# Kernel optimization log

Measured on AMD Instinct MI355X. Metric: run time of the kernel, lower is better.

Reference implementation:

```python
import jax, jax.numpy as jnp
import numpy as np

N, D, K = 8192, 4096, 8
F_HID = D // 4  # 1024


def setup_inputs() -> dict:
    key = jax.random.key(0)
    ks = jax.random.split(key, 8)
    s1 = 1.0 / np.sqrt(2 * D)
    s2 = 1.0 / np.sqrt(F_HID)
    sr = 1.0 / np.sqrt(D)
    return {
        "h_anchor": jax.random.normal(ks[0], (N, D), jnp.float32),
        "h_mask": jax.random.normal(ks[1], (N, D), jnp.float32),
        "Wr": jax.random.normal(ks[2], (K, D), jnp.float32) * sr,
        "br": jnp.zeros((K,), jnp.float32),
        "W1": jax.random.normal(ks[3], (K, F_HID, 2 * D), jnp.float32) * s1,
        "b1": jnp.zeros((K, F_HID), jnp.float32),
        "W2": jax.random.normal(ks[4], (K, D, F_HID), jnp.float32) * s2,
        "b2": jnp.zeros((K, D), jnp.float32),
    }


def reference(h_anchor, h_mask, Wr, br, W1, b1, W2, b2):
    # routing weights: softmax(h_mask @ Wr^T + br) -> [N, K]
    weights = jax.nn.softmax(h_mask @ Wr.T + br, axis=-1)
    # conditioned input: [N, 2D]
    conditioned = jnp.concatenate([h_anchor, h_mask], axis=-1)
    # all-expert first GEMM: [K, N, F]
    h1 = jnp.einsum("nc,kfc->knf", conditioned, W1) + b1[:, None, :]
    h1 = jax.nn.gelu(h1, approximate=False)  # torch nn.GELU default = exact erf
    # second GEMM: [K, N, D]
    expert_out = jnp.einsum("knf,kdf->knd", h1, W2) + b2[:, None, :]
    # softmax-weighted combine over experts -> [N, D]
    return jnp.einsum("knd,nk->nd", expert_out, weights)
```

## Files before the change

### kernel.cpp

```cpp
#include <hip/hip_runtime.h>
#include <hip/hip_bf16.h>
#include <math.h>

typedef __bf16 bf16_t;
typedef __bf16 bf16x4 __attribute__((ext_vector_type(4)));
typedef __bf16 bf16x8 __attribute__((ext_vector_type(8)));
typedef float  f32x4  __attribute__((ext_vector_type(4)));

#define AS1 __attribute__((address_space(1)))
#define AS3 __attribute__((address_space(3)))

__device__ __forceinline__ void gload_lds16(const bf16_t* g, char* l) {
  __builtin_amdgcn_global_load_lds((const AS1 void*)g, (AS3 void*)l, 16, 0, 0);
}

static constexpr int N_ROWS = 8192;
static constexpr int DDIM   = 4096;
static constexpr int KEXP   = 8;
static constexpr int FHID   = 1024;
static constexpr int KD     = 8192;
static constexpr int NKT64  = KD / 64;
static constexpr int NKT32  = KD / 32;


__global__ __launch_bounds__(256)
void routing_kernel(const float* __restrict__ hm, const float* __restrict__ Wr,
                    const float* __restrict__ br, float* __restrict__ wgt) {
  const int n = blockIdx.x;
  const int t = threadIdx.x;
  const int wid = t >> 6;
  const float4* row = (const float4*)(hm + (size_t)n * DDIM);
  float4 x[4];
#pragma unroll
  for (int j = 0; j < 4; ++j) x[j] = row[t + j * 256];
  __shared__ float red[KEXP][4];
  float part[KEXP];
#pragma unroll
  for (int k = 0; k < KEXP; ++k) {
    const float4* wr = (const float4*)(Wr + (size_t)k * DDIM);
    float s = 0.f;
#pragma unroll
    for (int j = 0; j < 4; ++j) {
      float4 w4 = wr[t + j * 256];
      s += x[j].x * w4.x + x[j].y * w4.y + x[j].z * w4.z + x[j].w * w4.w;
    }
#pragma unroll
    for (int off = 32; off > 0; off >>= 1) s += __shfl_down(s, off);
    part[k] = s;
  }
  if ((t & 63) == 0) {
#pragma unroll
    for (int k = 0; k < KEXP; ++k) red[k][wid] = part[k];
  }
  __syncthreads();
  if (t == 0) {
    float lg[KEXP];
    float mx = -1e30f;
#pragma unroll
    for (int k = 0; k < KEXP; ++k) {
      lg[k] = red[k][0] + red[k][1] + red[k][2] + red[k][3] + br[k];
      mx = fmaxf(mx, lg[k]);
    }
    float sum = 0.f;
#pragma unroll
    for (int k = 0; k < KEXP; ++k) { lg[k] = expf(lg[k] - mx); sum += lg[k]; }
    float inv = 1.f / sum;
#pragma unroll
    for (int k = 0; k < KEXP; ++k) wgt[(size_t)n * KEXP + k] = lg[k] * inv;
  }
}

__device__ __forceinline__ bf16x4 cvt4(float4 v) {
  bf16x4 o;
  o[0] = (bf16_t)v.x; o[1] = (bf16_t)v.y; o[2] = (bf16_t)v.z; o[3] = (bf16_t)v.w;
  return o;
}

__global__ __launch_bounds__(256)
void pack_cond_kernel(const float* __restrict__ ha, const float* __restrict__ hm,
                      bf16_t* __restrict__ Apk) {
  const int bm = blockIdx.x >> 7, t = blockIdx.x & 127;
  const int tid = threadIdx.x;
  const float* src = (t < 64) ? ha : hm;
  const int cb = (t & 63) * 64;
  __shared__ char pb[32768];
#pragma unroll
  for (int i = 0; i < 16; ++i) {
    int u = i * 256 + tid;
    int r = u >> 4, c = (u & 15) * 4;
    float4 v = *(const float4*)(src + (size_t)(bm * 256 + r) * DDIM + cb + c);
    int off = ((r >> 7) & 1) * 16384 + ((c >> 4) & 3) * 4096 + ((r >> 5) & 3) * 1024
            + ((c >> 3) & 1) * 512 + (r & 31) * 16 + (c & 7) * 2;
    *(bf16x4*)(pb + off) = cvt4(v);
  }
  __syncthreads();
  char* dst = (char*)Apk + (size_t)blockIdx.x * 32768;
#pragma unroll
  for (int i = 0; i < 8; ++i) {
    int off = i * 4096 + tid * 16;
    *(float4*)(dst + off) = *(const float4*)(pb + off);
  }
}

__global__ __launch_bounds__(256)
void pack_w1_kernel(const float* __restrict__ W1, bf16_t* __restrict__ Bpk) {
  const int bn = blockIdx.x >> 7, t = blockIdx.x & 127;
  const int tid = threadIdx.x;
  __shared__ char pb[32768];
#pragma unroll
  for (int i = 0; i < 16; ++i) {
    int u = i * 256 + tid;
    int r = u >> 4, c = (u & 15) * 4;
    float4 v = *(const float4*)(W1 + (size_t)(bn * 256 + r) * KD + t * 64 + c);
    int off = ((c >> 4) & 3) * 8192 + ((r >> 5) & 7) * 1024
            + ((c >> 3) & 1) * 512 + (r & 31) * 16 + (c & 7) * 2;
    *(bf16x4*)(pb + off) = cvt4(v);
  }
  __syncthreads();
  char* dst = (char*)Bpk + (size_t)blockIdx.x * 32768;
#pragma unroll
  for (int i = 0; i < 8; ++i) {
    int off = i * 4096 + tid * 16;
    *(float4*)(dst + off) = *(const float4*)(pb + off);
  }
}

__global__ __launch_bounds__(256)
void pack_w2_kernel(const float* __restrict__ W2, bf16_t* __restrict__ Bpk) {
  const int bn = blockIdx.x >> 7, t = blockIdx.x & 127;
  const int tid = threadIdx.x;
  const int ke = t >> 4, f0 = (t & 15) * 64;
  __shared__ char pb[32768];
#pragma unroll
  for (int i = 0; i < 16; ++i) {
    int u = i * 256 + tid;
    int r = u >> 4, c = (u & 15) * 4;
    float4 v = *(const float4*)(W2 + ((size_t)ke * DDIM + bn * 256 + r) * FHID + f0 + c);
    int off = ((c >> 4) & 3) * 8192 + ((r >> 5) & 7) * 1024
            + ((c >> 3) & 1) * 512 + (r & 31) * 16 + (c & 7) * 2;
    *(bf16x4*)(pb + off) = cvt4(v);
  }
  __syncthreads();
  char* dst = (char*)Bpk + (size_t)blockIdx.x * 32768;
#pragma unroll
  for (int i = 0; i < 8; ++i) {
    int off = i * 4096 + tid * 16;
    *(float4*)(dst + off) = *(const float4*)(pb + off);
  }
}

template <int MODE, int NCOLS>
__global__ __launch_bounds__(512, 4)
void gemm_kernel(const bf16_t* __restrict__ Apk, const bf16_t* __restrict__ Bpk,
                 void* __restrict__ Cout, const float* __restrict__ bias,
                 const float* __restrict__ wgt) {
  __shared__ char lds[3 * 24576];

  const int tid  = threadIdx.x;
  const int wid  = tid >> 6;
  const int lane = tid & 63;
  const int wr   = wid >> 1;
  const int wc   = wid & 1;

  constexpr int NBN    = NCOLS / 128;
  constexpr int NWIN_N = NBN / 16;
  const int bid = blockIdx.x;
  const int w   = bid >> 8;
  const int sl  = bid & 255;
  const int xcd = sl & 7;
  const int cu  = sl >> 3;
  const int wm  = w / NWIN_N, wn = w % NWIN_N;
  const int bm  = wm * 16 + ((xcd >> 1) << 2) + (cu & 3);
  const int bn  = wn * 16 + ((xcd & 1) << 3) + (cu >> 2);
  const int arow0 = bm * 256;
  const int bcol0 = bn * 128;

  const char* Abase = (const char*)Apk + (size_t)bm * NKT64 * 32768;
  const char* Bbase = (const char*)Bpk + (size_t)(bn >> 1) * NKT64 * 32768;
  const int pA0 = 2 * wid, pA1 = 2 * wid + 1, qB = wid;
  const int a0s = (pA0 >> 3) * 16384 + ((pA0 >> 2) & 1) * 4096 + (pA0 & 3) * 1024;
  const int a1s = (pA1 >> 3) * 16384 + ((pA1 >> 2) & 1) * 4096 + (pA1 & 3) * 1024;
  const int a0d = (pA0 >> 3) * 8192 + ((pA0 >> 2) & 1) * 4096 + (pA0 & 3) * 1024;
  const int a1d = (pA1 >> 3) * 8192 + ((pA1 >> 2) & 1) * 4096 + (pA1 & 3) * 1024;
  const int bqs = (qB >> 2) * 8192 + ((bn & 1) * 4 + (qB & 3)) * 1024;
  const int bqd = 16384 + (qB >> 2) * 4096 + (qB & 3) * 1024;

  const int lpart = (lane & 15) * 16 + ((lane >> 4) & 1) * 512 + (lane >> 5) * 4096;
  int aoff[4], boff[4];
#pragma unroll
  for (int mi = 0; mi < 4; ++mi)
    aoff[mi] = (wr >> 1) * 8192 + ((wr & 1) * 2 + (mi >> 1)) * 1024 + (mi & 1) * 256 + lpart;
#pragma unroll
  for (int nj = 0; nj < 4; ++nj)
    boff[nj] = 16384 + (wc * 2 + (nj >> 1)) * 1024 + (nj & 1) * 256 + lpart;

  f32x4 acc[4][4];
  f32x4 zero = {0.f, 0.f, 0.f, 0.f};
#pragma unroll
  for (int mi = 0; mi < 4; ++mi)
#pragma unroll
    for (int nj = 0; nj < 4; ++nj) acc[mi][nj] = zero;

#define SB __builtin_amdgcn_sched_barrier(0);
#define STG3(KT, BUF)                                                            \
  {                                                                              \
    const int kt_ = (KT) & (NKT32 - 1);                                          \
    const size_t t64 = (size_t)(kt_ >> 1) * 32768;                               \
    const int klo = (kt_ & 1) * 2;                                               \
    gload_lds16((const bf16_t*)(Abase + t64 + a0s + klo * 4096 + lane * 16),     \
                (BUF) + a0d);                                                    \
    gload_lds16((const bf16_t*)(Abase + t64 + a1s + klo * 4096 + lane * 16),     \
                (BUF) + a1d);                                                    \
    gload_lds16((const bf16_t*)(Bbase + t64 + bqs + klo * 8192 + lane * 16),     \
                (BUF) + bqd);                                                    \
  }

  STG3(0, lds) STG3(1, lds + 24576) SB
  asm volatile("s_waitcnt vmcnt(3)" ::: "memory");
  SB
  __builtin_amdgcn_s_barrier();
  SB

  char* rb = lds;
  char* mb = lds + 24576;
  char* sb = lds + 49152;

#pragma unroll 1
  for (int t = 0; t < NKT32; ++t) {
    STG3(t + 2, sb) SB
    bf16x8 a0, a1, a2, a3, b0, b1, b2, b3;
    a0 = *(const bf16x8*)(rb + aoff[0]); SB
    a1 = *(const bf16x8*)(rb + aoff[1]); SB
    a2 = *(const bf16x8*)(rb + aoff[2]); SB
    a3 = *(const bf16x8*)(rb + aoff[3]); SB
    b0 = *(const bf16x8*)(rb + boff[0]); SB
    b1 = *(const bf16x8*)(rb + boff[1]); SB
    b2 = *(const bf16x8*)(rb + boff[2]); SB
    b3 = *(const bf16x8*)(rb + boff[3]); SB
    __builtin_amdgcn_s_setprio(1);
    asm volatile("s_waitcnt lgkmcnt(3)" ::: "memory"); SB
    acc[0][0] = __builtin_amdgcn_mfma_f32_16x16x32_bf16(a0, b0, acc[0][0], 0, 0, 0);
    acc[1][0] = __builtin_amdgcn_mfma_f32_16x16x32_bf16(a1, b0, acc[1][0], 0, 0, 0);
    acc[2][0] = __builtin_amdgcn_mfma_f32_16x16x32_bf16(a2, b0, acc[2][0], 0, 0, 0);
    acc[3][0] = __builtin_amdgcn_mfma_f32_16x16x32_bf16(a3, b0, acc[3][0], 0, 0, 0);
    SB
    asm volatile("s_waitcnt lgkmcnt(2)" ::: "memory"); SB
    acc[0][1] = __builtin_amdgcn_mfma_f32_16x16x32_bf16(a0, b1, acc[0][1], 0, 0, 0);
    acc[1][1] = __builtin_amdgcn_mfma_f32_16x16x32_bf16(a1, b1, acc[1][1], 0, 0, 0);
    acc[2][1] = __builtin_amdgcn_mfma_f32_16x16x32_bf16(a2, b1, acc[2][1], 0, 0, 0);
    acc[3][1] = __builtin_amdgcn_mfma_f32_16x16x32_bf16(a3, b1, acc[3][1], 0, 0, 0);
    SB
    asm volatile("s_waitcnt lgkmcnt(1)" ::: "memory"); SB
    acc[0][2] = __builtin_amdgcn_mfma_f32_16x16x32_bf16(a0, b2, acc[0][2], 0, 0, 0);
    acc[1][2] = __builtin_amdgcn_mfma_f32_16x16x32_bf16(a1, b2, acc[1][2], 0, 0, 0);
    acc[2][2] = __builtin_amdgcn_mfma_f32_16x16x32_bf16(a2, b2, acc[2][2], 0, 0, 0);
    acc[3][2] = __builtin_amdgcn_mfma_f32_16x16x32_bf16(a3, b2, acc[3][2], 0, 0, 0);
    SB
    asm volatile("s_waitcnt lgkmcnt(0)" ::: "memory"); SB
    acc[0][3] = __builtin_amdgcn_mfma_f32_16x16x32_bf16(a0, b3, acc[0][3], 0, 0, 0);
    acc[1][3] = __builtin_amdgcn_mfma_f32_16x16x32_bf16(a1, b3, acc[1][3], 0, 0, 0);
    acc[2][3] = __builtin_amdgcn_mfma_f32_16x16x32_bf16(a2, b3, acc[2][3], 0, 0, 0);
    acc[3][3] = __builtin_amdgcn_mfma_f32_16x16x32_bf16(a3, b3, acc[3][3], 0, 0, 0);
    SB
    __builtin_amdgcn_s_setprio(0);
    asm volatile("s_waitcnt vmcnt(3)" ::: "memory");
    SB
    __builtin_amdgcn_s_barrier();
    SB
    char* tmp = rb; rb = mb; mb = sb; sb = tmp;
  }
#undef STG3
#undef SB

  const int rbase = arow0 + wr * 64 + ((lane >> 4) << 2);
  const int cbase = bcol0 + wc * 64 + (lane & 15);

  if constexpr (MODE == 1) {
    char* __restrict__ Hc = (char*)Cout;
    const int kexp = bcol0 >> 10;
    float bv[4];
    size_t cpart[4];
#pragma unroll
    for (int nj = 0; nj < 4; ++nj) {
      int c = cbase + nj * 16;
      bv[nj] = bias[c];
      cpart[nj] = (size_t)(c >> 6) * 32768 + ((c >> 4) & 3) * 4096
                + ((c >> 3) & 1) * 512 + (c & 7) * 2;
    }
#pragma unroll
    for (int mi = 0; mi < 4; ++mi)
#pragma unroll
      for (int r = 0; r < 4; ++r) {
        int n = rbase + mi * 16 + r;
        float wn4 = wgt[(size_t)n * KEXP + kexp];
        size_t npart = (size_t)(n >> 8) * (NKT64 * 32768) + ((n >> 7) & 1) * 16384
                     + ((n >> 5) & 3) * 1024 + (n & 31) * 16;
#pragma unroll
        for (int nj = 0; nj < 4; ++nj) {
          float x = acc[mi][nj][r] + bv[nj];
          float g = 0.5f * x * (1.f + erff(x * 0.70710678118654752f));
          *(bf16_t*)(Hc + npart + cpart[nj]) = (bf16_t)(g * wn4);
        }
      }
  } else {
    float* __restrict__ O = (float*)Cout;
    float bc[4][KEXP];
#pragma unroll
    for (int nj = 0; nj < 4; ++nj)
#pragma unroll
      for (int k = 0; k < KEXP; ++k)
        bc[nj][k] = bias[(size_t)k * NCOLS + cbase + nj * 16];
#pragma unroll
    for (int mi = 0; mi < 4; ++mi)
#pragma unroll
      for (int r = 0; r < 4; ++r) {
        int n = rbase + mi * 16 + r;
        const float4* wp = (const float4*)(wgt + (size_t)n * KEXP);
        float4 wa = wp[0], wb = wp[1];
        float w8[KEXP] = {wa.x, wa.y, wa.z, wa.w, wb.x, wb.y, wb.z, wb.w};
#pragma unroll
        for (int nj = 0; nj < 4; ++nj) {
          float s = 0.f;
#pragma unroll
          for (int k = 0; k < KEXP; ++k) s += w8[k] * bc[nj][k];
          O[(size_t)n * NCOLS + cbase + nj * 16] = acc[mi][nj][r] + s;
        }
      }
  }
}

extern "C" void kernel_launch(void* const* d_in, const int* in_sizes, int n_in,
                              void* d_out, int out_size, void* d_ws, size_t ws_size,
                              hipStream_t stream) {
  const float* h_anchor = (const float*)d_in[0];
  const float* h_mask   = (const float*)d_in[1];
  const float* Wr       = (const float*)d_in[2];
  const float* br       = (const float*)d_in[3];
  const float* W1       = (const float*)d_in[4];
  const float* b1       = (const float*)d_in[5];
  const float* W2       = (const float*)d_in[6];
  const float* b2       = (const float*)d_in[7];
  float* out = (float*)d_out;

  char* ws = (char*)d_ws;
  bf16_t* Apk  = (bf16_t*)(ws);
  bf16_t* B1pk = (bf16_t*)(ws + ((size_t)128 << 20));
  bf16_t* B2pk = (bf16_t*)(ws + ((size_t)256 << 20));
  bf16_t* Hpk  = (bf16_t*)(ws + ((size_t)320 << 20));
  float*  wgt  = (float*) (ws + ((size_t)448 << 20));

  routing_kernel<<<N_ROWS, 256, 0, stream>>>(h_mask, Wr, br, wgt);
  pack_cond_kernel<<<32 * 128, 256, 0, stream>>>(h_anchor, h_mask, Apk);
  pack_w1_kernel<<<32 * 128, 256, 0, stream>>>(W1, B1pk);
  pack_w2_kernel<<<16 * 128, 256, 0, stream>>>(W2, B2pk);

  gemm_kernel<1, 8192><<<(N_ROWS / 256) * (KD / 128), 512, 0, stream>>>(
      Apk, B1pk, (void*)Hpk, b1, wgt);
  gemm_kernel<2, 4096><<<(N_ROWS / 256) * (DDIM / 128), 512, 0, stream>>>(
      Hpk, B2pk, (void*)out, b2, wgt);
}
```

Baseline: 1.611 ms.

## Repack operands into contiguous K32 tiles and unroll triple-buffer loop

Changes the packed bf16 layout of activations and weights so that each 32-wide K step is one contiguous 16 KB chunk. Global-to-LDS loads can then use a single incrementing pointer instead of per-iteration address arithmetic. The main loop is unrolled by three with fixed LDS buffer offsets, which removes the buffer-pointer rotation and the per-thread offset arrays. The intent is to cut scalar and vector address overhead in the hot loop, at the cost of larger code and a layout change that the packing kernels and the hidden-activation epilogue must all match exactly.

```diff
diff --git a/kernel.cpp b/kernel.cpp
--- a/kernel.cpp
+++ b/kernel.cpp
@@ -19,7 +19,6 @@
 static constexpr int KEXP   = 8;
 static constexpr int FHID   = 1024;
 static constexpr int KD     = 8192;
-static constexpr int NKT64  = KD / 64;
 static constexpr int NKT32  = KD / 32;
 
 
@@ -89,8 +88,8 @@
     int u = i * 256 + tid;
     int r = u >> 4, c = (u & 15) * 4;
     float4 v = *(const float4*)(src + (size_t)(bm * 256 + r) * DDIM + cb + c);
-    int off = ((r >> 7) & 1) * 16384 + ((c >> 4) & 3) * 4096 + ((r >> 5) & 3) * 1024
-            + ((c >> 3) & 1) * 512 + (r & 31) * 16 + (c & 7) * 2;
+    int off = (c >> 5) * 16384 + ((r >> 7) & 1) * 8192 + ((c >> 4) & 1) * 4096
+            + ((r >> 5) & 3) * 1024 + ((c >> 3) & 1) * 512 + (r & 31) * 16 + (c & 7) * 2;
     *(bf16x4*)(pb + off) = cvt4(v);
   }
   __syncthreads();
@@ -112,7 +111,7 @@
     int u = i * 256 + tid;
     int r = u >> 4, c = (u & 15) * 4;
     float4 v = *(const float4*)(W1 + (size_t)(bn * 256 + r) * KD + t * 64 + c);
-    int off = ((c >> 4) & 3) * 8192 + ((r >> 5) & 7) * 1024
+    int off = (c >> 5) * 16384 + ((c >> 4) & 1) * 8192 + ((r >> 5) & 7) * 1024
             + ((c >> 3) & 1) * 512 + (r & 31) * 16 + (c & 7) * 2;
     *(bf16x4*)(pb + off) = cvt4(v);
   }
@@ -136,7 +135,7 @@
     int u = i * 256 + tid;
     int r = u >> 4, c = (u & 15) * 4;
     float4 v = *(const float4*)(W2 + ((size_t)ke * DDIM + bn * 256 + r) * FHID + f0 + c);
-    int off = ((c >> 4) & 3) * 8192 + ((r >> 5) & 7) * 1024
+    int off = (c >> 5) * 16384 + ((c >> 4) & 1) * 8192 + ((r >> 5) & 7) * 1024
             + ((c >> 3) & 1) * 512 + (r & 31) * 16 + (c & 7) * 2;
     *(bf16x4*)(pb + off) = cvt4(v);
   }
@@ -175,24 +174,17 @@
   const int arow0 = bm * 256;
   const int bcol0 = bn * 128;
 
-  const char* Abase = (const char*)Apk + (size_t)bm * NKT64 * 32768;
-  const char* Bbase = (const char*)Bpk + (size_t)(bn >> 1) * NKT64 * 32768;
-  const int pA0 = 2 * wid, pA1 = 2 * wid + 1, qB = wid;
-  const int a0s = (pA0 >> 3) * 16384 + ((pA0 >> 2) & 1) * 4096 + (pA0 & 3) * 1024;
-  const int a1s = (pA1 >> 3) * 16384 + ((pA1 >> 2) & 1) * 4096 + (pA1 & 3) * 1024;
-  const int a0d = (pA0 >> 3) * 8192 + ((pA0 >> 2) & 1) * 4096 + (pA0 & 3) * 1024;
-  const int a1d = (pA1 >> 3) * 8192 + ((pA1 >> 2) & 1) * 4096 + (pA1 & 3) * 1024;
-  const int bqs = (qB >> 2) * 8192 + ((bn & 1) * 4 + (qB & 3)) * 1024;
-  const int bqd = 16384 + (qB >> 2) * 4096 + (qB & 3) * 1024;
+  const int pA0 = 2 * wid, qB = wid;
+  const char* pA = (const char*)Apk + (size_t)bm * NKT32 * 16384
+                 + pA0 * 1024 + lane * 16;
+  const char* pB = (const char*)Bpk + (size_t)(bn >> 1) * NKT32 * 16384
+                 + (qB >> 2) * 8192 + ((bn & 1) * 4 + (qB & 3)) * 1024 + lane * 16;
+  const int dA = pA0 * 1024;
+  const int dB = 16384 + qB * 1024;
 
   const int lpart = (lane & 15) * 16 + ((lane >> 4) & 1) * 512 + (lane >> 5) * 4096;
-  int aoff[4], boff[4];
-#pragma unroll
-  for (int mi = 0; mi < 4; ++mi)
-    aoff[mi] = (wr >> 1) * 8192 + ((wr & 1) * 2 + (mi >> 1)) * 1024 + (mi & 1) * 256 + lpart;
-#pragma unroll
-  for (int nj = 0; nj < 4; ++nj)
-    boff[nj] = 16384 + (wc * 2 + (nj >> 1)) * 1024 + (nj & 1) * 256 + lpart;
+  const char* pAr = lds + (wr >> 1) * 8192 + (wr & 1) * 2048 + lpart;
+  const char* pBr = lds + 16384 + wc * 2048 + lpart;
 
   f32x4 acc[4][4];
   f32x4 zero = {0.f, 0.f, 0.f, 0.f};
@@ -202,74 +194,71 @@
     for (int nj = 0; nj < 4; ++nj) acc[mi][nj] = zero;
 
 #define SB __builtin_amdgcn_sched_barrier(0);
-#define STG3(KT, BUF)                                                            \
+#define STG(SBOFF)                                                               \
+  gload_lds16((const bf16_t*)pA,          lds + (SBOFF) + dA);                   \
+  gload_lds16((const bf16_t*)(pA + 1024), lds + (SBOFF) + dA + 1024);            \
+  gload_lds16((const bf16_t*)pB,          lds + (SBOFF) + dB);                   \
+  pA += 16384; pB += 16384;
+
+#define BODY(RB, SBOFF)                                                          \
   {                                                                              \
-    const int kt_ = (KT) & (NKT32 - 1);                                          \
-    const size_t t64 = (size_t)(kt_ >> 1) * 32768;                               \
-    const int klo = (kt_ & 1) * 2;                                               \
-    gload_lds16((const bf16_t*)(Abase + t64 + a0s + klo * 4096 + lane * 16),     \
-                (BUF) + a0d);                                                    \
-    gload_lds16((const bf16_t*)(Abase + t64 + a1s + klo * 4096 + lane * 16),     \
-                (BUF) + a1d);                                                    \
-    gload_lds16((const bf16_t*)(Bbase + t64 + bqs + klo * 8192 + lane * 16),     \
-                (BUF) + bqd);                                                    \
-  }
-
-  STG3(0, lds) STG3(1, lds + 24576) SB
+    STG(SBOFF) SB                                                                \
+    bf16x8 a0, a1, a2, a3, b0, b1, b2, b3;                                       \
+    a0 = *(const bf16x8*)(pAr + (RB));          SB                               \
+    a1 = *(const bf16x8*)(pAr + (RB) + 256);    SB                               \
+    a2 = *(const bf16x8*)(pAr + (RB) + 1024);   SB                               \
+    a3 = *(const bf16x8*)(pAr + (RB) + 1280);   SB                               \
+    b0 = *(const bf16x8*)(pBr + (RB));          SB                               \
+    b1 = *(const bf16x8*)(pBr + (RB) + 256);    SB                               \
+    b2 = *(const bf16x8*)(pBr + (RB) + 1024);   SB                               \
+    b3 = *(const bf16x8*)(pBr + (RB) + 1280);   SB                               \
+    __builtin_amdgcn_s_setprio(1);                                               \
+    asm volatile("s_waitcnt lgkmcnt(3)" ::: "memory"); SB                        \
+    acc[0][0] = __builtin_amdgcn_mfma_f32_16x16x32_bf16(a0, b0, acc[0][0], 0, 0, 0); \
+    acc[1][0] = __builtin_amdgcn_mfma_f32_16x16x32_bf16(a1, b0, acc[1][0], 0, 0, 0); \
+    acc[2][0] = __builtin_amdgcn_mfma_f32_16x16x32_bf16(a2, b0, acc[2][0], 0, 0, 0); \
+    acc[3][0] = __builtin_amdgcn_mfma_f32_16x16x32_bf16(a3, b0, acc[3][0], 0, 0, 0); \
+    SB                                                                           \
+    asm volatile("s_waitcnt lgkmcnt(2)" ::: "memory"); SB                        \
+    acc[0][1] = __builtin_amdgcn_mfma_f32_16x16x32_bf16(a0, b1, acc[0][1], 0, 0, 0); \
+    acc[1][1] = __builtin_amdgcn_mfma_f32_16x16x32_bf16(a1, b1, acc[1][1], 0, 0, 0); \
+    acc[2][1] = __builtin_amdgcn_mfma_f32_16x16x32_bf16(a2, b1, acc[2][1], 0, 0, 0); \
+    acc[3][1] = __builtin_amdgcn_mfma_f32_16x16x32_bf16(a3, b1, acc[3][1], 0, 0, 0); \
+    SB                                                                           \
+    asm volatile("s_waitcnt lgkmcnt(1)" ::: "memory"); SB                        \
+    acc[0][2] = __builtin_amdgcn_mfma_f32_16x16x32_bf16(a0, b2, acc[0][2], 0, 0, 0); \
+    acc[1][2] = __builtin_amdgcn_mfma_f32_16x16x32_bf16(a1, b2, acc[1][2], 0, 0, 0); \
+    acc[2][2] = __builtin_amdgcn_mfma_f32_16x16x32_bf16(a2, b2, acc[2][2], 0, 0, 0); \
+    acc[3][2] = __builtin_amdgcn_mfma_f32_16x16x32_bf16(a3, b2, acc[3][2], 0, 0, 0); \
+    SB                                                                           \
+    asm volatile("s_waitcnt lgkmcnt(0)" ::: "memory"); SB                        \
+    acc[0][3] = __builtin_amdgcn_mfma_f32_16x16x32_bf16(a0, b3, acc[0][3], 0, 0, 0); \
+    acc[1][3] = __builtin_amdgcn_mfma_f32_16x16x32_bf16(a1, b3, acc[1][3], 0, 0, 0); \
+    acc[2][3] = __builtin_amdgcn_mfma_f32_16x16x32_bf16(a2, b3, acc[2][3], 0, 0, 0); \
+    acc[3][3] = __builtin_amdgcn_mfma_f32_16x16x32_bf16(a3, b3, acc[3][3], 0, 0, 0); \
+    SB                                                                           \
+    __builtin_amdgcn_s_setprio(0);                                               \
+    asm volatile("s_waitcnt vmcnt(3)" ::: "memory");                             \
+    SB                                                                           \
+    __builtin_amdgcn_s_barrier();                                                \
+    SB                                                                           \
+  }
+
+  STG(0) STG(24576) SB
   asm volatile("s_waitcnt vmcnt(3)" ::: "memory");
   SB
   __builtin_amdgcn_s_barrier();
   SB
 
-  char* rb = lds;
-  char* mb = lds + 24576;
-  char* sb = lds + 49152;
-
 #pragma unroll 1
-  for (int t = 0; t < NKT32; ++t) {
-    STG3(t + 2, sb) SB
-    bf16x8 a0, a1, a2, a3, b0, b1, b2, b3;
-    a0 = *(const bf16x8*)(rb + aoff[0]); SB
-    a1 = *(const bf16x8*)(rb + aoff[1]); SB
-    a2 = *(const bf16x8*)(rb + aoff[2]); SB
-    a3 = *(const bf16x8*)(rb + aoff[3]); SB
-    b0 = *(const bf16x8*)(rb + boff[0]); SB
-    b1 = *(const bf16x8*)(rb + boff[1]); SB
-    b2 = *(const bf16x8*)(rb + boff[2]); SB
-    b3 = *(const bf16x8*)(rb + boff[3]); SB
-    __builtin_amdgcn_s_setprio(1);
-    asm volatile("s_waitcnt lgkmcnt(3)" ::: "memory"); SB
-    acc[0][0] = __builtin_amdgcn_mfma_f32_16x16x32_bf16(a0, b0, acc[0][0], 0, 0, 0);
-    acc[1][0] = __builtin_amdgcn_mfma_f32_16x16x32_bf16(a1, b0, acc[1][0], 0, 0, 0);
-    acc[2][0] = __builtin_amdgcn_mfma_f32_16x16x32_bf16(a2, b0, acc[2][0], 0, 0, 0);
-    acc[3][0] = __builtin_amdgcn_mfma_f32_16x16x32_bf16(a3, b0, acc[3][0], 0, 0, 0);
-    SB
-    asm volatile("s_waitcnt lgkmcnt(2)" ::: "memory"); SB
-    acc[0][1] = __builtin_amdgcn_mfma_f32_16x16x32_bf16(a0, b1, acc[0][1], 0, 0, 0);
-    acc[1][1] = __builtin_amdgcn_mfma_f32_16x16x32_bf16(a1, b1, acc[1][1], 0, 0, 0);
-    acc[2][1] = __builtin_amdgcn_mfma_f32_16x16x32_bf16(a2, b1, acc[2][1], 0, 0, 0);
-    acc[3][1] = __builtin_amdgcn_mfma_f32_16x16x32_bf16(a3, b1, acc[3][1], 0, 0, 0);
-    SB
-    asm volatile("s_waitcnt lgkmcnt(1)" ::: "memory"); SB
-    acc[0][2] = __builtin_amdgcn_mfma_f32_16x16x32_bf16(a0, b2, acc[0][2], 0, 0, 0);
-    acc[1][2] = __builtin_amdgcn_mfma_f32_16x16x32_bf16(a1, b2, acc[1][2], 0, 0, 0);
-    acc[2][2] = __builtin_amdgcn_mfma_f32_16x16x32_bf16(a2, b2, acc[2][2], 0, 0, 0);
-    acc[3][2] = __builtin_amdgcn_mfma_f32_16x16x32_bf16(a3, b2, acc[3][2], 0, 0, 0);
-    SB
-    asm volatile("s_waitcnt lgkmcnt(0)" ::: "memory"); SB
-    acc[0][3] = __builtin_amdgcn_mfma_f32_16x16x32_bf16(a0, b3, acc[0][3], 0, 0, 0);
-    acc[1][3] = __builtin_amdgcn_mfma_f32_16x16x32_bf16(a1, b3, acc[1][3], 0, 0, 0);
-    acc[2][3] = __builtin_amdgcn_mfma_f32_16x16x32_bf16(a2, b3, acc[2][3], 0, 0, 0);
-    acc[3][3] = __builtin_amdgcn_mfma_f32_16x16x32_bf16(a3, b3, acc[3][3], 0, 0, 0);
-    SB
-    __builtin_amdgcn_s_setprio(0);
-    asm volatile("s_waitcnt vmcnt(3)" ::: "memory");
-    SB
-    __builtin_amdgcn_s_barrier();
-    SB
-    char* tmp = rb; rb = mb; mb = sb; sb = tmp;
-  }
-#undef STG3
+  for (int it = 0; it < 85; ++it) {
+    BODY(0,     49152)
+    BODY(24576, 0)
+    BODY(49152, 24576)
+  }
+  BODY(0, 49152)
+#undef BODY
+#undef STG
 #undef SB
 
   const int rbase = arow0 + wr * 64 + ((lane >> 4) << 2);
@@ -284,7 +273,7 @@
     for (int nj = 0; nj < 4; ++nj) {
       int c = cbase + nj * 16;
       bv[nj] = bias[c];
-      cpart[nj] = (size_t)(c >> 6) * 32768 + ((c >> 4) & 3) * 4096
+      cpart[nj] = (size_t)(c >> 5) * 16384 + ((c >> 4) & 1) * 4096
                 + ((c >> 3) & 1) * 512 + (c & 7) * 2;
     }
 #pragma unroll
@@ -293,7 +282,7 @@
       for (int r = 0; r < 4; ++r) {
         int n = rbase + mi * 16 + r;
         float wn4 = wgt[(size_t)n * KEXP + kexp];
-        size_t npart = (size_t)(n >> 8) * (NKT64 * 32768) + ((n >> 7) & 1) * 16384
+        size_t npart = (size_t)(n >> 8) * (NKT32 * 16384) + ((n >> 7) & 1) * 8192
                      + ((n >> 5) & 3) * 1024 + (n & 31) * 16;
 #pragma unroll
         for (int nj = 0; nj < 4; ++nj) {
```

Result: faster. 1.542 ms (-4.3%).
